# Performance work log

Measured on AMD Instinct MI355X. Metric: run time of the kernel, lower is better.

Reference implementation:

```python
import jax, jax.numpy as jnp
import numpy as np

STACK = 1000            # stackSize (number of stacked TT networks, e.g. relations)
L = (8, 8, 8)           # input_fac[0]: left mode sizes  -> nRow = 512
R = (8, 8, 8)           # input_fac[1]: right mode sizes -> nCol = 512
RANKS = (16, 16)        # internal TT ranks (boundary ranks of 1 are dropped)
B = 512                 # batch of indices


def setup_inputs() -> dict:
    key = jax.random.key(0)
    k0, k1, k2, ki = jax.random.split(key, 4)
    # torch.rand(coreSize) * 0.1  ->  uniform[0, 0.1)
    core0 = jax.random.uniform(k0, (STACK, L[0], R[0], RANKS[0]), dtype=jnp.float32) * 0.1
    core1 = jax.random.uniform(k1, (STACK, RANKS[0], L[1], R[1], RANKS[1]), dtype=jnp.float32) * 0.1
    core2 = jax.random.uniform(k2, (STACK, RANKS[1], L[2], R[2]), dtype=jnp.float32) * 0.1
    indices = jax.random.randint(ki, (B,), 0, STACK, dtype=jnp.int64 if jax.config.read('jax_enable_x64') else jnp.int32)
    return {"core0": core0, "core1": core1, "core2": core2, "indices": indices}


def reference(core0, core1, core2, indices):
    # Gather the per-index TT cores
    c0 = core0[indices]  # [b, l0, r0, k1]
    c1 = core1[indices]  # [b, k1, l1, r1, k2]
    c2 = core2[indices]  # [b, k2, l2, r2]
    # Sequential TT-chain contraction over rank axes k1 then k2.
    # ncon out_order = [batch, l0, l1, l2, r0, r1, r2]
    t = jnp.einsum('baik,bkcjm->bacijm', c0, c1)        # [b, l0, l1, r0, r1, k2]
    out = jnp.einsum('bacijm,bmdl->bacdijl', t, c2)     # [b, l0, l1, l2, r0, r1, r2]
    nRow = L[0] * L[1] * L[2]
    nCol = R[0] * R[1] * R[2]
    return out.reshape(indices.shape[0], nRow, nCol)
```

## Files before the change

kernel.cpp:

```cpp
#include <hip/hip_runtime.h>
#include <stdint.h>


__device__ __forceinline__ float bflo(uint32_t u) { return __uint_as_float(u << 16); }
__device__ __forceinline__ float bfhi(uint32_t u) { return __uint_as_float(u & 0xffff0000u); }
__device__ __forceinline__ uint32_t pack_bf2(float f0, float f1) {
  uint32_t a = __float_as_uint(f0) + 0x8000u;
  uint32_t b = __float_as_uint(f1) + 0x8000u;
  return (a >> 16) | (b & 0xffff0000u);
}

__global__ __launch_bounds__(256) void tt_stack_kernel(
    const float* __restrict__ c0f,
    const float* __restrict__ c1f,
    const float* __restrict__ c2f,
    const int* __restrict__ idx,
    float* __restrict__ outf)
{
  __shared__ __align__(16) uint32_t lds_c1[8192];
  __shared__ __align__(16) float    lds_c0[128];
  __shared__ __align__(16) float    lds_c2[1024];
  __shared__ __align__(16) uint32_t lds_t[4096];

  const int tid = threadIdx.x;
  const int bid = blockIdx.x;
  const int b = bid >> 3;
  const int a = bid & 7;
  const int s = idx[b];

  {
    const float4* src4 = (const float4*)(c1f + (size_t)s * 16384);
#pragma unroll
    for (int r = 0; r < 16; ++r) {
      const float4 v = src4[r * 256 + tid];
      uint2* dst = (uint2*)&lds_c1[2 * (r * 256 + tid)];
      *dst = make_uint2(pack_bf2(v.x, v.y), pack_bf2(v.z, v.w));
    }
  }
  if (tid < 128) lds_c0[tid] = c0f[(size_t)(s * 8 + a) * 128 + tid];
#pragma unroll
  for (int r = 0; r < 4; ++r) lds_c2[r * 256 + tid] = c2f[(size_t)s * 1024 + r * 256 + tid];
  __syncthreads();

#pragma unroll
  for (int cc = 0; cc < 2; ++cc) {
    const int combo = tid + cc * 256;
    const int c = combo >> 6;
    const int i = (combo >> 3) & 7;
    const int j = combo & 7;
    float a_k[16];
#pragma unroll
    for (int k = 0; k < 16; ++k) a_k[k] = lds_c0[i * 16 + k];
    float acc[16];
#pragma unroll
    for (int m = 0; m < 16; ++m) acc[m] = 0.f;
#pragma unroll
    for (int k = 0; k < 16; ++k) {
      const uint4* rp = (const uint4*)&lds_c1[((k * 8 + c) * 8 + j) * 8];
      const uint4 u0 = rp[0];
      const uint4 u1 = rp[1];
      const float av = a_k[k];
      acc[0]  = fmaf(av, bflo(u0.x), acc[0]);   acc[1]  = fmaf(av, bfhi(u0.x), acc[1]);
      acc[2]  = fmaf(av, bflo(u0.y), acc[2]);   acc[3]  = fmaf(av, bfhi(u0.y), acc[3]);
      acc[4]  = fmaf(av, bflo(u0.z), acc[4]);   acc[5]  = fmaf(av, bfhi(u0.z), acc[5]);
      acc[6]  = fmaf(av, bflo(u0.w), acc[6]);   acc[7]  = fmaf(av, bfhi(u0.w), acc[7]);
      acc[8]  = fmaf(av, bflo(u1.x), acc[8]);   acc[9]  = fmaf(av, bfhi(u1.x), acc[9]);
      acc[10] = fmaf(av, bflo(u1.y), acc[10]);  acc[11] = fmaf(av, bfhi(u1.y), acc[11]);
      acc[12] = fmaf(av, bflo(u1.z), acc[12]);  acc[13] = fmaf(av, bfhi(u1.z), acc[13]);
      acc[14] = fmaf(av, bflo(u1.w), acc[14]);  acc[15] = fmaf(av, bfhi(u1.w), acc[15]);
    }
    uint4* tp = (uint4*)&lds_t[combo * 8];
    tp[0] = make_uint4(pack_bf2(acc[0],  acc[1]),  pack_bf2(acc[2],  acc[3]),
                       pack_bf2(acc[4],  acc[5]),  pack_bf2(acc[6],  acc[7]));
    tp[1] = make_uint4(pack_bf2(acc[8],  acc[9]),  pack_bf2(acc[10], acc[11]),
                       pack_bf2(acc[12], acc[13]), pack_bf2(acc[14], acc[15]));
  }
  __syncthreads();

  const int g = tid & 15;
  const int d = g >> 1;
  const int lh = g & 1;
  const int set = tid >> 4;
  float c2r[16][4];
#pragma unroll
  for (int m = 0; m < 16; ++m) {
    const float4 v = *(const float4*)&lds_c2[m * 64 + d * 8 + lh * 4];
    c2r[m][0] = v.x; c2r[m][1] = v.y; c2r[m][2] = v.z; c2r[m][3] = v.w;
  }
  float* outb = outf + (size_t)b * 262144 + (size_t)a * 32768;
  for (int rr = 0; rr < 32; ++rr) {
    const int row = rr * 16 + set;
    const int c = row >> 6;
    const int i = (row >> 3) & 7;
    const int j = row & 7;
    const uint4* tp = (const uint4*)&lds_t[row * 8];
    const uint4 t0 = tp[0];
    const uint4 t1 = tp[1];
    float tm[16];
    tm[0]=bflo(t0.x); tm[1]=bfhi(t0.x); tm[2]=bflo(t0.y); tm[3]=bfhi(t0.y);
    tm[4]=bflo(t0.z); tm[5]=bfhi(t0.z); tm[6]=bflo(t0.w); tm[7]=bfhi(t0.w);
    tm[8]=bflo(t1.x); tm[9]=bfhi(t1.x); tm[10]=bflo(t1.y); tm[11]=bfhi(t1.y);
    tm[12]=bflo(t1.z); tm[13]=bfhi(t1.z); tm[14]=bflo(t1.w); tm[15]=bfhi(t1.w);
    float acc4[4] = {0.f, 0.f, 0.f, 0.f};
#pragma unroll
    for (int m = 0; m < 16; ++m) {
      acc4[0] = fmaf(tm[m], c2r[m][0], acc4[0]);
      acc4[1] = fmaf(tm[m], c2r[m][1], acc4[1]);
      acc4[2] = fmaf(tm[m], c2r[m][2], acc4[2]);
      acc4[3] = fmaf(tm[m], c2r[m][3], acc4[3]);
    }
    float4* dst = (float4*)(outb + ((c * 8 + d) << 9) + i * 64 + j * 8 + lh * 4);
    *dst = make_float4(acc4[0], acc4[1], acc4[2], acc4[3]);
  }
}

extern "C" void kernel_launch(void* const* d_in, const int* in_sizes, int n_in,
                              void* d_out, int out_size, void* d_ws, size_t ws_size,
                              hipStream_t stream) {
  const float* c0f = (const float*)d_in[0];
  const float* c1f = (const float*)d_in[1];
  const float* c2f = (const float*)d_in[2];
  const int* idx = (const int*)d_in[3];
  float* outf = (float*)d_out;
  const int B = in_sizes[3];
  dim3 grid(B * 8), block(256);
  hipLaunchKernelGGL(tt_stack_kernel, grid, block, 0, stream, c0f, c1f, c2f, idx, outf);
}
```

Baseline: 608.0 us.

## Use MFMA for second TT contraction and process all rows per block

Each block now handles one batch index with 512 threads and loops over all 8 l0 values, so the c1 core is gathered and converted to bf16 once instead of eight times. The second contraction against core2 uses bf16 16x16x32 MFMA, with core2 split into hi/lo bf16 halves so the rank-16 reduction keeps near-fp32 precision. This removes redundant global loads and scalar FMA work, but output stores become scattered scalar writes instead of float4 stores. The lds_t buffer is also reused across iterations without a barrier.

```diff
diff --git a/kernel.cpp b/kernel.cpp
--- a/kernel.cpp
+++ b/kernel.cpp
@@ -1,6 +1,9 @@
 #include <hip/hip_runtime.h>
 #include <stdint.h>
 
+
+typedef short short8 __attribute__((ext_vector_type(8)));
+typedef float f32x4 __attribute__((ext_vector_type(4)));
 
 __device__ __forceinline__ float bflo(uint32_t u) { return __uint_as_float(u << 16); }
 __device__ __forceinline__ float bfhi(uint32_t u) { return __uint_as_float(u & 0xffff0000u); }
@@ -10,7 +13,7 @@
   return (a >> 16) | (b & 0xffff0000u);
 }
 
-__global__ __launch_bounds__(256) void tt_stack_kernel(
+__global__ __launch_bounds__(512, 4) void tt_stack_kernel(
     const float* __restrict__ c0f,
     const float* __restrict__ c1f,
     const float* __restrict__ c2f,
@@ -18,39 +21,61 @@
     float* __restrict__ outf)
 {
   __shared__ __align__(16) uint32_t lds_c1[8192];
-  __shared__ __align__(16) float    lds_c0[128];
-  __shared__ __align__(16) float    lds_c2[1024];
+  __shared__ __align__(16) float    lds_c0[1024];
+  __shared__ __align__(16) uint32_t lds_c2b[1024];
   __shared__ __align__(16) uint32_t lds_t[4096];
 
   const int tid = threadIdx.x;
-  const int bid = blockIdx.x;
-  const int b = bid >> 3;
-  const int a = bid & 7;
+  const int b = blockIdx.x;
   const int s = idx[b];
+  const size_t s1024 = (size_t)s * 1024;
 
   {
     const float4* src4 = (const float4*)(c1f + (size_t)s * 16384);
+    float4 cv[8];
 #pragma unroll
-    for (int r = 0; r < 16; ++r) {
-      const float4 v = src4[r * 256 + tid];
-      uint2* dst = (uint2*)&lds_c1[2 * (r * 256 + tid)];
-      *dst = make_uint2(pack_bf2(v.x, v.y), pack_bf2(v.z, v.w));
+    for (int it = 0; it < 8; ++it) cv[it] = src4[it * 512 + tid];
+    const float g0 = c0f[s1024 + tid];
+    const float g1 = c0f[s1024 + 512 + tid];
+    const int w = tid & 7;
+    const int col = tid >> 3;
+    const float v0 = c2f[s1024 + (size_t)(2 * w) * 64 + col];
+    const float v1 = c2f[s1024 + (size_t)(2 * w + 1) * 64 + col];
+#pragma unroll
+    for (int it = 0; it < 8; ++it) {
+      uint2* dst = (uint2*)&lds_c1[2 * (it * 512 + tid)];
+      *dst = make_uint2(pack_bf2(cv[it].x, cv[it].y), pack_bf2(cv[it].z, cv[it].w));
     }
+    lds_c0[tid] = g0;
+    lds_c0[512 + tid] = g1;
+    const uint32_t h0 = (__float_as_uint(v0) + 0x8000u) & 0xffff0000u;
+    const uint32_t h1 = (__float_as_uint(v1) + 0x8000u) & 0xffff0000u;
+    lds_c2b[col * 16 + w] = (h0 >> 16) | h1;
+    lds_c2b[col * 16 + 8 + w] =
+        pack_bf2(v0 - __uint_as_float(h0), v1 - __uint_as_float(h1));
   }
-  if (tid < 128) lds_c0[tid] = c0f[(size_t)(s * 8 + a) * 128 + tid];
-#pragma unroll
-  for (int r = 0; r < 4; ++r) lds_c2[r * 256 + tid] = c2f[(size_t)s * 1024 + r * 256 + tid];
   __syncthreads();
 
+  const int lane = tid & 63, wv = tid >> 6;
+  const int g = lane >> 4, lcol = lane & 15;
+
+  short8 Bfr[4];
 #pragma unroll
-  for (int cc = 0; cc < 2; ++cc) {
-    const int combo = tid + cc * 256;
-    const int c = combo >> 6;
-    const int i = (combo >> 3) & 7;
-    const int j = combo & 7;
+  for (int ct = 0; ct < 4; ++ct)
+    Bfr[ct] = *(const short8*)&lds_c2b[(ct * 16 + lcol) * 16 + g * 4];
+
+  const int c = tid >> 6, i = (tid >> 3) & 7, j = tid & 7;
+  const int sw = (tid >> 2) & 1;
+  const int hsel = (g & 1) ^ ((lcol >> 2) & 1);
+  float* const outb = outf + (size_t)b * 262144;
+
+  for (int a = 0; a < 8; ++a) {
     float a_k[16];
+    {
+      const float4* c0p = (const float4*)&lds_c0[a * 128 + i * 16];
 #pragma unroll
-    for (int k = 0; k < 16; ++k) a_k[k] = lds_c0[i * 16 + k];
+      for (int q = 0; q < 4; ++q) *(float4*)&a_k[q * 4] = c0p[q];
+    }
     float acc[16];
 #pragma unroll
     for (int m = 0; m < 16; ++m) acc[m] = 0.f;
@@ -69,48 +94,36 @@
       acc[12] = fmaf(av, bflo(u1.z), acc[12]);  acc[13] = fmaf(av, bfhi(u1.z), acc[13]);
       acc[14] = fmaf(av, bflo(u1.w), acc[14]);  acc[15] = fmaf(av, bfhi(u1.w), acc[15]);
     }
-    uint4* tp = (uint4*)&lds_t[combo * 8];
-    tp[0] = make_uint4(pack_bf2(acc[0],  acc[1]),  pack_bf2(acc[2],  acc[3]),
-                       pack_bf2(acc[4],  acc[5]),  pack_bf2(acc[6],  acc[7]));
-    tp[1] = make_uint4(pack_bf2(acc[8],  acc[9]),  pack_bf2(acc[10], acc[11]),
-                       pack_bf2(acc[12], acc[13]), pack_bf2(acc[14], acc[15]));
-  }
-  __syncthreads();
+    {
+      uint32_t* tb = &lds_t[tid * 8];
+      *(uint4*)&tb[sw * 4] =
+          make_uint4(pack_bf2(acc[0], acc[1]),  pack_bf2(acc[2], acc[3]),
+                     pack_bf2(acc[4], acc[5]),  pack_bf2(acc[6], acc[7]));
+      *(uint4*)&tb[4 - sw * 4] =
+          make_uint4(pack_bf2(acc[8], acc[9]),  pack_bf2(acc[10], acc[11]),
+                     pack_bf2(acc[12], acc[13]), pack_bf2(acc[14], acc[15]));
+    }
 
-  const int g = tid & 15;
-  const int d = g >> 1;
-  const int lh = g & 1;
-  const int set = tid >> 4;
-  float c2r[16][4];
+    float* const oa = outb + a * 32768;
 #pragma unroll
-  for (int m = 0; m < 16; ++m) {
-    const float4 v = *(const float4*)&lds_c2[m * 64 + d * 8 + lh * 4];
-    c2r[m][0] = v.x; c2r[m][1] = v.y; c2r[m][2] = v.z; c2r[m][3] = v.w;
-  }
-  float* outb = outf + (size_t)b * 262144 + (size_t)a * 32768;
-  for (int rr = 0; rr < 32; ++rr) {
-    const int row = rr * 16 + set;
-    const int c = row >> 6;
-    const int i = (row >> 3) & 7;
-    const int j = row & 7;
-    const uint4* tp = (const uint4*)&lds_t[row * 8];
-    const uint4 t0 = tp[0];
-    const uint4 t1 = tp[1];
-    float tm[16];
-    tm[0]=bflo(t0.x); tm[1]=bfhi(t0.x); tm[2]=bflo(t0.y); tm[3]=bfhi(t0.y);
-    tm[4]=bflo(t0.z); tm[5]=bfhi(t0.z); tm[6]=bflo(t0.w); tm[7]=bfhi(t0.w);
-    tm[8]=bflo(t1.x); tm[9]=bfhi(t1.x); tm[10]=bflo(t1.y); tm[11]=bfhi(t1.y);
-    tm[12]=bflo(t1.z); tm[13]=bfhi(t1.z); tm[14]=bflo(t1.w); tm[15]=bfhi(t1.w);
-    float acc4[4] = {0.f, 0.f, 0.f, 0.f};
+    for (int rt4 = 0; rt4 < 4; ++rt4) {
+      const int rt = wv * 4 + rt4;
+      const int row = rt * 16 + lcol;
+      const short8 av8 = *(const short8*)&lds_t[row * 8 + hsel * 4];
+      const int ii = (rt * 2 + (g >> 1)) & 7;
+      float* const ob = oa + (rt >> 2) * 4096 + ii * 64 + (g & 1) * 32;
 #pragma unroll
-    for (int m = 0; m < 16; ++m) {
-      acc4[0] = fmaf(tm[m], c2r[m][0], acc4[0]);
-      acc4[1] = fmaf(tm[m], c2r[m][1], acc4[1]);
-      acc4[2] = fmaf(tm[m], c2r[m][2], acc4[2]);
-      acc4[3] = fmaf(tm[m], c2r[m][3], acc4[3]);
+      for (int ct = 0; ct < 4; ++ct) {
+        f32x4 dd = {0.f, 0.f, 0.f, 0.f};
+        dd = __builtin_amdgcn_mfma_f32_16x16x32_bf16(av8, Bfr[ct], dd, 0, 0, 0);
+        const int colx = ct * 16 + lcol;
+        float* p = ob + ((colx >> 3) * 512) + (colx & 7);
+        p[0]  = dd[0];
+        p[8]  = dd[1];
+        p[16] = dd[2];
+        p[24] = dd[3];
+      }
     }
-    float4* dst = (float4*)(outb + ((c * 8 + d) << 9) + i * 64 + j * 8 + lh * 4);
-    *dst = make_float4(acc4[0], acc4[1], acc4[2], acc4[3]);
   }
 }
 
@@ -123,6 +136,6 @@
   const int* idx = (const int*)d_in[3];
   float* outf = (float*)d_out;
   const int B = in_sizes[3];
-  dim3 grid(B * 8), block(256);
+  dim3 grid(B), block(512);
   hipLaunchKernelGGL(tt_stack_kernel, grid, block, 0, stream, c0f, c1f, c2f, idx, outf);
 }
```

Result: slower. 936.0 us (+53.9%).
